# Optimization experiments

Hardware: AMD Instinct MI355X
Metric: run time of the kernel (lower is better)

## Reference

```python
import jax, jax.numpy as jnp
import numpy as np

N, L, C, NHEAD = 4, 2048, 1024, 8
D = C // NHEAD
EPS_ATTN = 1e-6
EPS_LN = 1e-5


def _w(key, shape, scale=0.02):
    return jax.random.normal(key, shape, dtype=jnp.float32) * scale


def setup_inputs() -> dict:
    key = jax.random.key(0)
    ks = jax.random.split(key, 32)
    inp = {
        'depth_feat': jax.random.normal(ks[0], (N, L, C), dtype=jnp.float32),
        'context_feat': jax.random.normal(ks[1], (N, L, C), dtype=jnp.float32),
        'depth_pos': jax.random.normal(ks[2], (N, L, C), dtype=jnp.float32),
        # encoder params (weights stored [in, out]; y = x @ W)
        'e_wq': _w(ks[3], (C, C)), 'e_wk': _w(ks[4], (C, C)), 'e_wv': _w(ks[5], (C, C)),
        'e_wm': _w(ks[6], (C, C)),
        'e_w1': _w(ks[7], (C, 2 * C)), 'e_w2': _w(ks[8], (2 * C, C)),
        'e_g1': jnp.ones((C,), jnp.float32), 'e_b1': jnp.zeros((C,), jnp.float32),
        'e_g2': jnp.ones((C,), jnp.float32), 'e_b2': jnp.zeros((C,), jnp.float32),
        # decoder params
        'd_wq0': _w(ks[9], (C, C)), 'd_wk0': _w(ks[10], (C, C)), 'd_wv0': _w(ks[11], (C, C)),
        'd_wm0': _w(ks[12], (C, C)),
        'd_wq1': _w(ks[13], (C, C)), 'd_wk1': _w(ks[14], (C, C)), 'd_wv1': _w(ks[15], (C, C)),
        'd_wm1': _w(ks[16], (C, C)),
        'd_w1': _w(ks[17], (C, 2 * C)), 'd_w2': _w(ks[18], (2 * C, C)),
        'd_g0': jnp.ones((C,), jnp.float32), 'd_b0': jnp.zeros((C,), jnp.float32),
        'd_g1': jnp.ones((C,), jnp.float32), 'd_b1': jnp.zeros((C,), jnp.float32),
        'd_g2': jnp.ones((C,), jnp.float32), 'd_b2': jnp.zeros((C,), jnp.float32),
    }
    return inp


def layernorm(x, g, b):
    m = jnp.mean(x, axis=-1, keepdims=True)
    v = jnp.mean(jnp.square(x - m), axis=-1, keepdims=True)
    return (x - m) * jax.lax.rsqrt(v + EPS_LN) * g + b


def linear_attention(q, k, v):
    # q,k,v: [N, L, H, D]; elu+1 feature map, O(L) kernelized attention
    Q = jax.nn.elu(q) + 1.0
    K = jax.nn.elu(k) + 1.0
    vlen = v.shape[1]
    v = v / vlen
    KV = jnp.einsum('nshd,nshv->nhdv', K, v)                    # [N,H,D,D]
    Z = 1.0 / (jnp.einsum('nlhd,nhd->nlh', Q, K.sum(axis=1)) + EPS_ATTN)
    out = jnp.einsum('nlhd,nhdv,nlh->nlhv', Q, KV, Z) * vlen    # [N,L,H,D]
    return out


def heads(x):
    n, l, c = x.shape
    return x.reshape(n, l, NHEAD, D)


def encoder_layer(x, wq, wk, wv, wm, w1, w2, g1, b1, g2, b2):
    n, l, c = x.shape
    msg = linear_attention(heads(x @ wq), heads(x @ wk), heads(x @ wv))
    msg = msg.reshape(n, l, c) @ wm
    x = x + layernorm(msg, g1, b1)
    x = x + layernorm(jax.nn.relu(x @ w1) @ w2, g2, b2)
    return x


def decoder_layer(x, src, wq0, wk0, wv0, wm0, wq1, wk1, wv1, wm1, w1, w2, g0, b0, g1, b1, g2, b2):
    n, l, c = x.shape
    msg = linear_attention(heads(x @ wq0), heads(x @ wk0), heads(x @ wv0))
    msg = msg.reshape(n, l, c) @ wm0
    x = x + layernorm(msg, g0, b0)
    msg = linear_attention(heads(x @ wq1), heads(src @ wk1), heads(src @ wv1))
    msg = msg.reshape(n, l, c) @ wm1
    x = x + layernorm(msg, g1, b1)
    x = x + layernorm(jax.nn.relu(x @ w1) @ w2, g2, b2)
    return x


def reference(depth_feat, context_feat, depth_pos,
              e_wq, e_wk, e_wv, e_wm, e_w1, e_w2, e_g1, e_b1, e_g2, e_b2,
              d_wq0, d_wk0, d_wv0, d_wm0, d_wq1, d_wk1, d_wv1, d_wm1,
              d_w1, d_w2, d_g0, d_b0, d_g1, d_b1, d_g2, d_b2):
    ctx = context_feat + depth_pos
    ctx = encoder_layer(ctx, e_wq, e_wk, e_wv, e_wm, e_w1, e_w2, e_g1, e_b1, e_g2, e_b2)
    out = decoder_layer(depth_feat, ctx,
                        d_wq0, d_wk0, d_wv0, d_wm0,
                        d_wq1, d_wk1, d_wv1, d_wm1,
                        d_w1, d_w2, d_g0, d_b0, d_g1, d_b1, d_g2, d_b2)
    return out
```

## Files before the change

kernel.cpp:

```cpp
#include <hip/hip_runtime.h>
#include <cstdint>

#define N_B 4
#define L_S 2048
#define C_F 1024
#define H_N 8
#define D_H 128
#define M_T (N_B * L_S)

typedef __bf16 bf16;
typedef __bf16 bf16x4 __attribute__((ext_vector_type(4)));
typedef __bf16 bf16x8 __attribute__((ext_vector_type(8)));
typedef float f32x4 __attribute__((ext_vector_type(4)));

typedef __attribute__((address_space(1))) void gvoid_t;
typedef __attribute__((address_space(3))) void lvoid_t;

__device__ __forceinline__ void lds_cp16(void* lds, const void* g) {
    __builtin_amdgcn_global_load_lds((gvoid_t*)g, (lvoid_t*)lds, 16, 0, 0);
}

__device__ __forceinline__ float elup1(float x) {
    return x > 0.0f ? x + 1.0f : __expf(x);
}

__device__ __forceinline__ void load4f(const void* base, size_t e0, int isbf, float* o) {
    if (isbf) {
        bf16x4 v = *(const bf16x4*)((const bf16*)base + e0);
        o[0] = (float)v[0]; o[1] = (float)v[1]; o[2] = (float)v[2]; o[3] = (float)v[3];
    } else {
        float4 v = *(const float4*)((const float*)base + e0);
        o[0] = v.x; o[1] = v.y; o[2] = v.z; o[3] = v.w;
    }
}

__global__ void detect_dtype(const unsigned int* g1, int* flag) {
    if (threadIdx.x == 0 && blockIdx.x == 0)
        *flag = (g1[0] == 0x3F803F80u) ? 1 : 0;
}

__global__ __launch_bounds__(256) void transpose_any(
        const void* __restrict__ src, bf16* __restrict__ dst,
        int R, int Cc, const int* __restrict__ flagp) {
    const int isbf = *flagp;
    __shared__ bf16 tile[32][33];
    const int bx = blockIdx.x * 32;
    const int by = blockIdx.y * 32;
    const int tx = threadIdx.x & 31;
    const int ty = threadIdx.x >> 5;
#pragma unroll
    for (int i = 0; i < 32; i += 8) {
        size_t ix = (size_t)(by + ty + i) * Cc + bx + tx;
        float v = isbf ? (float)((const bf16*)src)[ix] : ((const float*)src)[ix];
        tile[ty + i][tx] = (bf16)v;
    }
    __syncthreads();
#pragma unroll
    for (int i = 0; i < 32; i += 8)
        dst[(size_t)(bx + ty + i) * R + by + tx] = tile[tx][ty + i];
}

struct TAll {
    const void* src[16];
    unsigned int dstoff[16];
    int R[16];
    int C[16];
    int tile0[17];
};

__global__ __launch_bounds__(256) void transpose_all(
        TAll p, bf16* __restrict__ twall, const int* __restrict__ flagp) {
    const int isbf = *flagp;
    int gid = blockIdx.x;
    int w = 0;
    while (gid >= p.tile0[w + 1]) ++w;
    const int local = gid - p.tile0[w];
    const int R = p.R[w], Cc = p.C[w];
    const int tilesx = Cc >> 5;
    const int bx = (local % tilesx) * 32;
    const int by = (local / tilesx) * 32;
    const void* src = p.src[w];
    bf16* dst = twall + p.dstoff[w];
    __shared__ bf16 tile[32][33];
    const int tx = threadIdx.x & 31;
    const int ty = threadIdx.x >> 5;
#pragma unroll
    for (int i = 0; i < 32; i += 8) {
        size_t ix = (size_t)(by + ty + i) * Cc + bx + tx;
        float v = isbf ? (float)((const bf16*)src)[ix] : ((const float*)src)[ix];
        tile[ty + i][tx] = (bf16)v;
    }
    __syncthreads();
#pragma unroll
    for (int i = 0; i < 32; i += 8)
        dst[(size_t)(bx + ty + i) * R + by + tx] = tile[tx][ty + i];
}

template <int ACT>
__global__ __launch_bounds__(256, 2) void gemm_bt(
        const bf16* __restrict__ A, const bf16* __restrict__ Bt,
        bf16* __restrict__ C, int M, int N, int K) {
    __shared__ bf16 sA[128 * 64];
    __shared__ bf16 sB[128 * 64];
    const int t = threadIdx.x;
    const int lane = t & 63;
    const int w = t >> 6;
    const int wm = (w >> 1) * 64, wn = (w & 1) * 64;
    const int lr = lane & 15, lq = lane >> 4;
    const int m0 = blockIdx.y * 128, n0 = blockIdx.x * 128;

    f32x4 acc[4][4] = {};

    for (int kt = 0; kt < K; kt += 64) {
        const bf16* Ag = A + (size_t)m0 * K + kt;
        const bf16* Bg = Bt + (size_t)n0 * K + kt;
#pragma unroll
        for (int i = 0; i < 4; ++i) {
            int ci = t + i * 256;
            int r = ci >> 3, c8 = (ci & 7) * 8;
            lds_cp16(&sA[ci * 8], Ag + (size_t)r * K + c8);
        }
#pragma unroll
        for (int i = 0; i < 4; ++i) {
            int ci = t + i * 256;
            int r = ci >> 3, c8 = (ci & 7) * 8;
            lds_cp16(&sB[ci * 8], Bg + (size_t)r * K + c8);
        }
        __syncthreads();
#pragma unroll
        for (int kk = 0; kk < 64; kk += 32) {
            bf16x8 af[4], bfr[4];
#pragma unroll
            for (int mi = 0; mi < 4; ++mi)
                af[mi] = *(const bf16x8*)&sA[(wm + mi * 16 + lr) * 64 + kk + lq * 8];
#pragma unroll
            for (int ni = 0; ni < 4; ++ni)
                bfr[ni] = *(const bf16x8*)&sB[(wn + ni * 16 + lr) * 64 + kk + lq * 8];
#pragma unroll
            for (int mi = 0; mi < 4; ++mi)
#pragma unroll
                for (int ni = 0; ni < 4; ++ni)
                    acc[mi][ni] = __builtin_amdgcn_mfma_f32_16x16x32_bf16(
                        af[mi], bfr[ni], acc[mi][ni], 0, 0, 0);
        }
        __syncthreads();
    }
#pragma unroll
    for (int mi = 0; mi < 4; ++mi)
#pragma unroll
        for (int ni = 0; ni < 4; ++ni)
#pragma unroll
            for (int r = 0; r < 4; ++r) {
                int row = m0 + wm + mi * 16 + lq * 4 + r;
                int col = n0 + wn + ni * 16 + lr;
                float v = acc[mi][ni][r];
                if (ACT == 1) v = fmaxf(v, 0.0f);
                if (ACT == 2) v = v > 0.0f ? v + 1.0f : __expf(v);
                C[(size_t)row * N + col] = (bf16)v;
            }
}

#define STAGE_T(sarr, Gbase, ldstride, Tt)                                    \
    {                                                                         \
        const int sl_ = (Tt) & 3;                                             \
        _Pragma("unroll")                                                     \
        for (int i_ = 0; i_ < 2; ++i_) {                                      \
            int ci_ = t + i_ * 512;                                           \
            int r_ = ci_ >> 2, c8_ = (ci_ & 3) * 8;                           \
            lds_cp16(&sarr[sl_ * 8192 + ci_ * 8],                             \
                     (Gbase) + (size_t)r_ * (ldstride) + ((Tt) << 5) +        \
                         (c8_ ^ ((r_ & 3) << 3)));                            \
        }                                                                     \
    }

template <int ACT>
__global__ __launch_bounds__(512, 2) void gemm256(
        const bf16* __restrict__ A, const bf16* __restrict__ Bt,
        bf16* __restrict__ C, int M, int N, int K, int actsplit) {
    __shared__ bf16 sA[4 * 256 * 32];
    __shared__ bf16 sB[4 * 256 * 32];
    const int t = threadIdx.x;
    const int lane = t & 63;
    const int w = t >> 6;
    const int wr = w >> 2, wc = w & 3;
    const int lr = lane & 15, lq = lane >> 4;
    const int m0 = blockIdx.y * 256, n0 = blockIdx.x * 256;
    const int nt = K >> 5;

    const bf16* Ab = A + (size_t)m0 * K;
    const bf16* Bb = Bt + (size_t)n0 * K;

    f32x4 acc[8][4] = {};

    STAGE_T(sA, Ab, K, 0); STAGE_T(sB, Bb, K, 0);
    STAGE_T(sA, Ab, K, 1); STAGE_T(sB, Bb, K, 1);
    asm volatile("s_waitcnt vmcnt(4)" ::: "memory");
    __builtin_amdgcn_s_barrier();

    for (int T = 0; T < nt; ++T) {
        const bf16* sAs = &sA[(T & 3) * 8192];
        const bf16* sBs = &sB[(T & 3) * 8192];
        bf16x8 af[4], bfr[4], ag[4];
#pragma unroll
        for (int mi = 0; mi < 4; ++mi) {
            int row = wr * 128 + mi * 16 + lr;
            af[mi] = *(const bf16x8*)&sAs[row * 32 + ((lq * 8) ^ ((row & 3) << 3))];
        }
#pragma unroll
        for (int ni = 0; ni < 4; ++ni) {
            int row = wc * 64 + ni * 16 + lr;
            bfr[ni] = *(const bf16x8*)&sBs[row * 32 + ((lq * 8) ^ ((row & 3) << 3))];
        }
        if (T + 2 < nt) STAGE_T(sA, Ab, K, T + 2);
        __builtin_amdgcn_s_barrier();
        __builtin_amdgcn_s_setprio(1);
#pragma unroll
        for (int mi = 0; mi < 4; ++mi)
#pragma unroll
            for (int ni = 0; ni < 4; ++ni)
                acc[mi][ni] = __builtin_amdgcn_mfma_f32_16x16x32_bf16(
                    af[mi], bfr[ni], acc[mi][ni], 0, 0, 0);
        __builtin_amdgcn_s_setprio(0);
        __builtin_amdgcn_s_barrier();
#pragma unroll
        for (int mi = 0; mi < 4; ++mi) {
            int row = wr * 128 + (mi + 4) * 16 + lr;
            ag[mi] = *(const bf16x8*)&sAs[row * 32 + ((lq * 8) ^ ((row & 3) << 3))];
        }
        if (T + 2 < nt) STAGE_T(sB, Bb, K, T + 2);
        __builtin_amdgcn_s_barrier();
        __builtin_amdgcn_s_setprio(1);
#pragma unroll
        for (int mi = 0; mi < 4; ++mi)
#pragma unroll
            for (int ni = 0; ni < 4; ++ni)
                acc[mi + 4][ni] = __builtin_amdgcn_mfma_f32_16x16x32_bf16(
                    ag[mi], bfr[ni], acc[mi + 4][ni], 0, 0, 0);
        __builtin_amdgcn_s_setprio(0);
        if (T + 1 < nt) {
            if (T + 2 < nt) asm volatile("s_waitcnt vmcnt(4)" ::: "memory");
            else            asm volatile("s_waitcnt vmcnt(0)" ::: "memory");
        }
        __builtin_amdgcn_s_barrier();
    }
#pragma unroll
    for (int mi = 0; mi < 8; ++mi)
#pragma unroll
        for (int ni = 0; ni < 4; ++ni)
#pragma unroll
            for (int r = 0; r < 4; ++r) {
                int row = m0 + wr * 128 + mi * 16 + lq * 4 + r;
                int col = n0 + wc * 64 + ni * 16 + lr;
                float v = acc[mi][ni][r];
                if (ACT == 1) v = fmaxf(v, 0.0f);
                if (ACT == 3 && row < actsplit) v = v > 0.0f ? v + 1.0f : __expf(v);
                C[(size_t)row * N + col] = (bf16)v;
            }
}

__global__ __launch_bounds__(256, 2) void attn_kv_mfma(
        const bf16* __restrict__ ktg, const bf16* __restrict__ vtg,
        bf16* __restrict__ KVp, float* __restrict__ KSp) {
    const int nh = blockIdx.x;
    const int chunk = blockIdx.y;
    const int n = nh >> 3, h = nh & 7;
    const int t = threadIdx.x;
    const int lane = t & 63;
    const int w = t >> 6;
    const int wm = (w >> 1) * 64, wn = (w & 1) * 64;
    const int lr = lane & 15, lq = lane >> 4;
    __shared__ bf16 sA[128 * 64];
    __shared__ bf16 sB[128 * 64];
    const size_t base = (size_t)(h * D_H) * M_T + (size_t)n * L_S + chunk * 128;

    f32x4 acc[4][4] = {};
    float ks = 0.0f;
    const int dh = t >> 1, half = (t & 1) * 32;

    for (int kt = 0; kt < 128; kt += 64) {
        const bf16* Ag = vtg + base + kt;
        const bf16* Bg = ktg + base + kt;
#pragma unroll
        for (int i = 0; i < 4; ++i) {
            int ci = t + i * 256;
            int r = ci >> 3, c8 = (ci & 7) * 8;
            lds_cp16(&sA[ci * 8], Ag + (size_t)r * M_T + c8);
        }
#pragma unroll
        for (int i = 0; i < 4; ++i) {
            int ci = t + i * 256;
            int r = ci >> 3, c8 = (ci & 7) * 8;
            lds_cp16(&sB[ci * 8], Bg + (size_t)r * M_T + c8);
        }
        __syncthreads();
#pragma unroll
        for (int j = 0; j < 4; ++j) {
            bf16x8 v = *(const bf16x8*)&sB[dh * 64 + half + j * 8];
#pragma unroll
            for (int m = 0; m < 8; ++m) ks += (float)v[m];
        }
#pragma unroll
        for (int kk = 0; kk < 64; kk += 32) {
            bf16x8 af[4], bfr[4];
#pragma unroll
            for (int mi = 0; mi < 4; ++mi)
                af[mi] = *(const bf16x8*)&sA[(wm + mi * 16 + lr) * 64 + kk + lq * 8];
#pragma unroll
            for (int ni = 0; ni < 4; ++ni)
                bfr[ni] = *(const bf16x8*)&sB[(wn + ni * 16 + lr) * 64 + kk + lq * 8];
#pragma unroll
            for (int mi = 0; mi < 4; ++mi)
#pragma unroll
                for (int ni = 0; ni < 4; ++ni)
                    acc[mi][ni] = __builtin_amdgcn_mfma_f32_16x16x32_bf16(
                        af[mi], bfr[ni], acc[mi][ni], 0, 0, 0);
        }
        __syncthreads();
    }
    float ko = __shfl_xor(ks, 1);
    if (!(t & 1)) KSp[(nh * 16 + chunk) * D_H + dh] = ks + ko;

    bf16* out = KVp + ((size_t)(nh * 16 + chunk)) * (D_H * D_H);
#pragma unroll
    for (int mi = 0; mi < 4; ++mi)
#pragma unroll
        for (int ni = 0; ni < 4; ++ni)
#pragma unroll
            for (int r = 0; r < 4; ++r) {
                int row = wm + mi * 16 + lq * 4 + r;
                int col = wn + ni * 16 + lr;
                out[(size_t)row * D_H + col] = (bf16)acc[mi][ni][r];
            }
}

__global__ __launch_bounds__(256) void attn_reduce_t(
        const bf16* __restrict__ KVp, const float* __restrict__ KSp,
        bf16* __restrict__ KVt, float* __restrict__ Ksum) {
    const int nh = blockIdx.x;
    const int es = blockIdx.y;
    const int t = threadIdx.x;
    const size_t base = (size_t)nh * 16 * (D_H * D_H) + es * 4096 + t * 16;
    float fa[16] = {};
    for (int c = 0; c < 16; ++c) {
        const bf16* p = KVp + base + (size_t)c * (D_H * D_H);
        bf16x8 a = *(const bf16x8*)p;
        bf16x8 b = *(const bf16x8*)(p + 8);
#pragma unroll
        for (int m = 0; m < 8; ++m) { fa[m] += (float)a[m]; fa[8 + m] += (float)b[m]; }
    }
    bf16* o = KVt + (size_t)nh * (D_H * D_H) + es * 4096 + t * 16;
    bf16x8 oa, ob;
#pragma unroll
    for (int m = 0; m < 8; ++m) { oa[m] = (bf16)fa[m]; ob[m] = (bf16)fa[8 + m]; }
    *(bf16x8*)o = oa;
    *(bf16x8*)(o + 8) = ob;
    if (es == 0 && t < 128) {
        float s = 0.0f;
#pragma unroll
        for (int c = 0; c < 16; ++c) s += KSp[(nh * 16 + c) * D_H + t];
        Ksum[nh * D_H + t] = s;
    }
}

__global__ __launch_bounds__(256, 2) void attn_out_mfma(
        const bf16* __restrict__ qb, const bf16* __restrict__ KVt,
        const float* __restrict__ Ksum, bf16* __restrict__ ab) {
    const int nh = blockIdx.x, tile = blockIdx.y;
    const int n = nh >> 3, h = nh & 7;
    const int t = threadIdx.x;
    const int lane = t & 63;
    const int w = t >> 6;
    const int wm = (w >> 1) * 64, wn = (w & 1) * 64;
    const int lr = lane & 15, lq = lane >> 4;
    __shared__ bf16 sA[128 * 64];
    __shared__ bf16 sB[128 * 64];
    __shared__ float sKs[128];
    __shared__ float sZp[128][2];
    __shared__ float sZ[128];
    if (t < 128) sKs[t] = Ksum[nh * D_H + t];

    f32x4 acc[4][4] = {};
    float zacc = 0.0f;
    const int zrow = t >> 1, zoff = (t & 1) * 32;
    const size_t qbase = ((size_t)(n * L_S + tile * 128)) * C_F + h * D_H;

    for (int kt = 0; kt < 128; kt += 64) {
        __syncthreads();
#pragma unroll
        for (int i = 0; i < 4; ++i) {
            int ci = t + i * 256;
            int r = ci >> 3, c8 = (ci & 7) * 8;
            lds_cp16(&sA[ci * 8], qb + qbase + (size_t)r * C_F + kt + c8);
            lds_cp16(&sB[ci * 8], KVt + (size_t)nh * (D_H * D_H) + (size_t)r * D_H + kt + c8);
        }
        __syncthreads();
#pragma unroll 8
        for (int j = 0; j < 32; ++j)
            zacc += (float)sA[zrow * 64 + zoff + j] * sKs[kt + zoff + j];
#pragma unroll
        for (int kk = 0; kk < 64; kk += 32) {
            bf16x8 af[4], bfr[4];
#pragma unroll
            for (int mi = 0; mi < 4; ++mi)
                af[mi] = *(const bf16x8*)&sA[(wm + mi * 16 + lr) * 64 + kk + lq * 8];
#pragma unroll
            for (int ni = 0; ni < 4; ++ni)
                bfr[ni] = *(const bf16x8*)&sB[(wn + ni * 16 + lr) * 64 + kk + lq * 8];
#pragma unroll
            for (int mi = 0; mi < 4; ++mi)
#pragma unroll
                for (int ni = 0; ni < 4; ++ni)
                    acc[mi][ni] = __builtin_amdgcn_mfma_f32_16x16x32_bf16(
                        af[mi], bfr[ni], acc[mi][ni], 0, 0, 0);
        }
    }
    sZp[zrow][t & 1] = zacc;
    __syncthreads();
    if (t < 128) sZ[t] = 1.0f / (sZp[t][0] + sZp[t][1] + 1e-6f);
    __syncthreads();
#pragma unroll
    for (int mi = 0; mi < 4; ++mi)
#pragma unroll
        for (int ni = 0; ni < 4; ++ni)
#pragma unroll
            for (int r = 0; r < 4; ++r) {
                int row = wm + mi * 16 + lq * 4 + r;
                int col = wn + ni * 16 + lr;
                ab[qbase + (size_t)row * C_F + col] = (bf16)(acc[mi][ni][r] * sZ[row]);
            }
}

template <int F32OUT>
__global__ __launch_bounds__(256) void ln_res(
        const bf16* __restrict__ msg, const void* __restrict__ g,
        const void* __restrict__ bb, const int* __restrict__ flagp,
        const bf16* __restrict__ xin, void* __restrict__ xout) {
    const int isbf = *flagp;
    const int row = blockIdx.x * 4 + (threadIdx.x >> 6);
    const int lane = threadIdx.x & 63;
    const size_t base = (size_t)row * C_F;
    float m[16];
#pragma unroll
    for (int k = 0; k < 4; ++k) {
        bf16x4 v = *(const bf16x4*)(msg + base + k * 256 + lane * 4);
        m[k * 4 + 0] = (float)v[0]; m[k * 4 + 1] = (float)v[1];
        m[k * 4 + 2] = (float)v[2]; m[k * 4 + 3] = (float)v[3];
    }
    float s1 = 0.0f, s2 = 0.0f;
#pragma unroll
    for (int q = 0; q < 16; ++q) { s1 += m[q]; s2 += m[q] * m[q]; }
#pragma unroll
    for (int off = 32; off > 0; off >>= 1) {
        s1 += __shfl_down(s1, off);
        s2 += __shfl_down(s2, off);
    }
    s1 = __shfl(s1, 0);
    s2 = __shfl(s2, 0);
    const float mean = s1 / C_F;
    const float rs = rsqrtf(s2 / C_F - mean * mean + 1e-5f);
#pragma unroll
    for (int k = 0; k < 4; ++k) {
        const size_t cix = k * 256 + lane * 4;
        float ga[4], ba[4];
        load4f(g, cix, isbf, ga);
        load4f(bb, cix, isbf, ba);
        bf16x4 x4 = *(const bf16x4*)(xin + base + cix);
        if (F32OUT) {
            float4 of;
            of.x = (float)x4[0] + (m[k * 4 + 0] - mean) * rs * ga[0] + ba[0];
            of.y = (float)x4[1] + (m[k * 4 + 1] - mean) * rs * ga[1] + ba[1];
            of.z = (float)x4[2] + (m[k * 4 + 2] - mean) * rs * ga[2] + ba[2];
            of.w = (float)x4[3] + (m[k * 4 + 3] - mean) * rs * ga[3] + ba[3];
            *(float4*)((float*)xout + base + cix) = of;
        } else {
            bf16x4 ob;
            ob[0] = (bf16)((float)x4[0] + (m[k * 4 + 0] - mean) * rs * ga[0] + ba[0]);
            ob[1] = (bf16)((float)x4[1] + (m[k * 4 + 1] - mean) * rs * ga[1] + ba[1]);
            ob[2] = (bf16)((float)x4[2] + (m[k * 4 + 2] - mean) * rs * ga[2] + ba[2]);
            ob[3] = (bf16)((float)x4[3] + (m[k * 4 + 3] - mean) * rs * ga[3] + ba[3]);
            *(bf16x4*)((bf16*)xout + base + cix) = ob;
        }
    }
}

__global__ __launch_bounds__(256) void init_ctx_kernel(
        const void* __restrict__ a, const void* __restrict__ b,
        const int* __restrict__ flagp, bf16* __restrict__ xb) {
    const int isbf = *flagp;
    const size_t i = ((size_t)blockIdx.x * 256 + threadIdx.x) * 4;
    float av[4], bv[4];
    load4f(a, i, isbf, av);
    load4f(b, i, isbf, bv);
    bf16x4 o;
#pragma unroll
    for (int q = 0; q < 4; ++q) o[q] = (bf16)(av[q] + bv[q]);
    *(bf16x4*)(xb + i) = o;
}

__global__ __launch_bounds__(256) void conv_copy_kernel(
        const void* __restrict__ a, const int* __restrict__ flagp,
        bf16* __restrict__ xb) {
    const int isbf = *flagp;
    const size_t i = ((size_t)blockIdx.x * 256 + threadIdx.x) * 4;
    float av[4];
    load4f(a, i, isbf, av);
    bf16x4 o;
#pragma unroll
    for (int q = 0; q < 4; ++q) o[q] = (bf16)av[q];
    *(bf16x4*)(xb + i) = o;
}

extern "C" void kernel_launch(void* const* d_in, const int* in_sizes, int n_in,
                              void* d_out, int out_size, void* d_ws, size_t ws_size,
                              hipStream_t stream) {
    const size_t MB = 1u << 20;
    uint8_t* W = (uint8_t*)d_ws;
    bf16* xb    = (bf16*)(W + 0);
    bf16* ctxb  = (bf16*)(W + 16 * MB);
    bf16* qb    = (bf16*)(W + 32 * MB);
    bf16* kb    = (bf16*)(W + 48 * MB);
    bf16* vb    = (bf16*)(W + 64 * MB);
    bf16* hb    = kb;
    bf16* S     = (bf16*)(W + 80 * MB);
    bf16* TW    = (bf16*)(W + 96 * MB);
    bf16* KVp   = S;
    float* KSp  = (float*)(W + 100 * MB);
    bf16* KVt   = (bf16*)(W + 101 * MB);
    float* Ksum = (float*)(W + 102 * MB);
    int*   flag = (int*)(W + 102 * MB + 64 * 1024);
    bf16* TWall = (bf16*)(W + 104 * MB);
    const bool batched = (ws_size >= 145 * MB);

    detect_dtype<<<1, 64, 0, stream>>>((const unsigned int*)d_in[9], flag);

    const int widx[16] = {3,4,5,6,7,8,13,14,15,16,17,18,19,20,21,22};
    const int wR[16]   = {1024,1024,1024,1024,1024,2048,1024,1024,1024,1024,
                          1024,1024,1024,1024,1024,2048};
    const int wC[16]   = {1024,1024,1024,1024,2048,1024,1024,1024,1024,1024,
                          1024,1024,1024,1024,2048,1024};
    unsigned int off[16];
    {
        unsigned int acc = 0;
        for (int i = 0; i < 16; ++i) { off[i] = acc; acc += (unsigned int)wR[i] * wC[i]; }
    }
    if (batched) {
        TAll p;
        int tacc = 0;
        for (int i = 0; i < 16; ++i) {
            p.src[i] = d_in[widx[i]];
            p.dstoff[i] = off[i];
            p.R[i] = wR[i];
            p.C[i] = wC[i];
            p.tile0[i] = tacc;
            tacc += (wR[i] / 32) * (wC[i] / 32);
        }
        p.tile0[16] = tacc;
        transpose_all<<<tacc, 256, 0, stream>>>(p, TWall, flag);
    }
    auto SLOT = [&](int idx) {
        for (int i = 0; i < 16; ++i) if (widx[i] == idx) return i;
        return 0;
    };
    auto BT = [&](int idx) -> const bf16* {
        int s = SLOT(idx);
        if (batched) return TWall + off[s];
        dim3 g(wC[s] / 32, wR[s] / 32);
        transpose_any<<<g, 256, 0, stream>>>(d_in[idx], TW, wR[s], wC[s], flag);
        return TW;
    };
    auto TG = [&](int idx, const bf16* A, bf16* Cc, int Nn, int Kk, int act) {
        const bf16* Bt = BT(idx);
        dim3 g(Nn / 128, M_T / 128);
        if (act == 1)      gemm_bt<1><<<g, 256, 0, stream>>>(A, Bt, Cc, M_T, Nn, Kk);
        else if (act == 2) gemm_bt<2><<<g, 256, 0, stream>>>(A, Bt, Cc, M_T, Nn, Kk);
        else               gemm_bt<0><<<g, 256, 0, stream>>>(A, Bt, Cc, M_T, Nn, Kk);
    };
    auto KVF = [&](int kidx, int vidx, const bf16* X) {
        const bf16* Wt;
        if (batched) {
            Wt = TWall + off[SLOT(kidx)];
        } else {
            dim3 g(32, 32);
            transpose_any<<<g, 256, 0, stream>>>(d_in[kidx], TW, 1024, 1024, flag);
            transpose_any<<<g, 256, 0, stream>>>(d_in[vidx], TW + 1024 * 1024, 1024, 1024, flag);
            Wt = TW;
        }
        dim3 g(M_T / 256, (2 * C_F) / 256);
        gemm256<3><<<g, 512, 0, stream>>>(Wt, X, kb, 2 * C_F, M_T, C_F, C_F);
    };
    auto FFN1 = [&](int idx, const bf16* A) {
        const bf16* Bt = BT(idx);
        dim3 g((2 * C_F) / 256, M_T / 256);
        gemm256<1><<<g, 512, 0, stream>>>(A, Bt, hb, M_T, 2 * C_F, C_F, 0);
    };
    auto ATT = [&](const bf16* q, const bf16* k, const bf16* v, bf16* o) {
        attn_kv_mfma<<<dim3(32, 16), 256, 0, stream>>>(k, v, KVp, KSp);
        attn_reduce_t<<<dim3(32, 4), 256, 0, stream>>>(KVp, KSp, KVt, Ksum);
        attn_out_mfma<<<dim3(32, 16), 256, 0, stream>>>(q, KVt, Ksum, o);
    };
    auto LN = [&](const bf16* m, int gi, int bi, const bf16* xi, bf16* xo) {
        ln_res<0><<<M_T / 4, 256, 0, stream>>>(m, d_in[gi], d_in[bi], flag, xi, (void*)xo);
    };

    init_ctx_kernel<<<M_T * C_F / 1024, 256, 0, stream>>>(d_in[1], d_in[2], flag, xb);
    TG(3, xb, qb, C_F, C_F, 2);
    KVF(4, 5, xb);
    ATT(qb, kb, vb, S);
    TG(6, S, qb, C_F, C_F, 0);
    LN(qb, 9, 10, xb, xb);
    FFN1(7, xb);
    TG(8, hb, S, C_F, 2 * C_F, 0);
    LN(S, 11, 12, xb, ctxb);

    conv_copy_kernel<<<M_T * C_F / 1024, 256, 0, stream>>>(d_in[0], flag, xb);
    TG(13, xb, qb, C_F, C_F, 2);
    KVF(14, 15, xb);
    ATT(qb, kb, vb, S);
    TG(16, S, qb, C_F, C_F, 0);
    LN(qb, 23, 24, xb, xb);
    TG(17, xb, qb, C_F, C_F, 2);
    KVF(18, 19, ctxb);
    ATT(qb, kb, vb, S);
    TG(20, S, qb, C_F, C_F, 0);
    LN(qb, 25, 26, xb, xb);
    FFN1(21, xb);
    TG(22, hb, S, C_F, 2 * C_F, 0);
    ln_res<1><<<M_T / 4, 256, 0, stream>>>(S, d_in[27], d_in[28], flag, xb, d_out);
}
```

Measured before the change: 867.3 us.

## Replace 256-tile pipelined GEMM with 128x64 tiles and XCD-aware tile remap

Removes the 256x256 multi-stage pipelined GEMM and routes the KV-projection and FFN1 GEMMs through the simpler 128x128 kernel. N=1024 GEMMs now use a new 128x64-tile kernel that allows 4 blocks per CU. A tile_map function remaps workgroup IDs so neighbouring tiles land on the same XCD, aiming for better L2 reuse and more blocks in flight. The cost is losing the software-pipelined, LDS-swizzled 256 kernel, which may have had higher MFMA efficiency on the large GEMMs.

Result: slower. 927.7 us (+7.0%).

```diff
diff --git a/kernel.cpp b/kernel.cpp
--- a/kernel.cpp
+++ b/kernel.cpp
@@ -32,6 +32,18 @@
         float4 v = *(const float4*)((const float*)base + e0);
         o[0] = v.x; o[1] = v.y; o[2] = v.z; o[3] = v.w;
     }
+}
+
+__device__ __forceinline__ void tile_map(int orig, int gx, int gy,
+                                         int* mtile, int* ntile) {
+    const int nwg = gx * gy;
+    const int q = nwg >> 3;
+    const int s = (orig & 7) * q + (orig >> 3);
+    const int G = gx << 3;
+    const int g = s / G;
+    const int r = s - g * G;
+    *ntile = r >> 3;
+    *mtile = g * 8 + (r & 7);
 }
 
 __global__ void detect_dtype(const unsigned int* g1, int* flag) {
@@ -99,7 +111,7 @@
 template <int ACT>
 __global__ __launch_bounds__(256, 2) void gemm_bt(
         const bf16* __restrict__ A, const bf16* __restrict__ Bt,
-        bf16* __restrict__ C, int M, int N, int K) {
+        bf16* __restrict__ C, int M, int N, int K, int actsplit) {
     __shared__ bf16 sA[128 * 64];
     __shared__ bf16 sB[128 * 64];
     const int t = threadIdx.x;
@@ -107,24 +119,27 @@
     const int w = t >> 6;
     const int wm = (w >> 1) * 64, wn = (w & 1) * 64;
     const int lr = lane & 15, lq = lane >> 4;
-    const int m0 = blockIdx.y * 128, n0 = blockIdx.x * 128;
+    int mt, nt_;
+    tile_map(blockIdx.y * gridDim.x + blockIdx.x, gridDim.x, gridDim.y, &mt, &nt_);
+    const int m0 = mt * 128, n0 = nt_ * 128;
+
+    const bf16* Ab = A + (size_t)m0 * K;
+    const bf16* Bb = Bt + (size_t)n0 * K;
 
     f32x4 acc[4][4] = {};
 
     for (int kt = 0; kt < K; kt += 64) {
-        const bf16* Ag = A + (size_t)m0 * K + kt;
-        const bf16* Bg = Bt + (size_t)n0 * K + kt;
 #pragma unroll
         for (int i = 0; i < 4; ++i) {
             int ci = t + i * 256;
             int r = ci >> 3, c8 = (ci & 7) * 8;
-            lds_cp16(&sA[ci * 8], Ag + (size_t)r * K + c8);
+            lds_cp16(&sA[ci * 8], Ab + (size_t)r * K + kt + c8);
         }
 #pragma unroll
         for (int i = 0; i < 4; ++i) {
             int ci = t + i * 256;
             int r = ci >> 3, c8 = (ci & 7) * 8;
-            lds_cp16(&sB[ci * 8], Bg + (size_t)r * K + c8);
+            lds_cp16(&sB[ci * 8], Bb + (size_t)r * K + kt + c8);
         }
         __syncthreads();
 #pragma unroll
@@ -156,104 +171,74 @@
                 float v = acc[mi][ni][r];
                 if (ACT == 1) v = fmaxf(v, 0.0f);
                 if (ACT == 2) v = v > 0.0f ? v + 1.0f : __expf(v);
+                if (ACT == 3 && row < actsplit) v = v > 0.0f ? v + 1.0f : __expf(v);
                 C[(size_t)row * N + col] = (bf16)v;
             }
 }
 
-#define STAGE_T(sarr, Gbase, ldstride, Tt)                                    \
-    {                                                                         \
-        const int sl_ = (Tt) & 3;                                             \
-        _Pragma("unroll")                                                     \
-        for (int i_ = 0; i_ < 2; ++i_) {                                      \
-            int ci_ = t + i_ * 512;                                           \
-            int r_ = ci_ >> 2, c8_ = (ci_ & 3) * 8;                           \
-            lds_cp16(&sarr[sl_ * 8192 + ci_ * 8],                             \
-                     (Gbase) + (size_t)r_ * (ldstride) + ((Tt) << 5) +        \
-                         (c8_ ^ ((r_ & 3) << 3)));                            \
-        }                                                                     \
-    }
-
 template <int ACT>
-__global__ __launch_bounds__(512, 2) void gemm256(
+__global__ __launch_bounds__(256, 4) void gemm_bn64(
         const bf16* __restrict__ A, const bf16* __restrict__ Bt,
-        bf16* __restrict__ C, int M, int N, int K, int actsplit) {
-    __shared__ bf16 sA[4 * 256 * 32];
-    __shared__ bf16 sB[4 * 256 * 32];
+        bf16* __restrict__ C, int M, int N, int K) {
+    __shared__ bf16 sA[128 * 64];
+    __shared__ bf16 sB[64 * 64];
     const int t = threadIdx.x;
     const int lane = t & 63;
     const int w = t >> 6;
-    const int wr = w >> 2, wc = w & 3;
+    const int wm = (w >> 1) * 64, wn = (w & 1) * 32;
     const int lr = lane & 15, lq = lane >> 4;
-    const int m0 = blockIdx.y * 256, n0 = blockIdx.x * 256;
-    const int nt = K >> 5;
+    int mt, nt_;
+    tile_map(blockIdx.y * gridDim.x + blockIdx.x, gridDim.x, gridDim.y, &mt, &nt_);
+    const int m0 = mt * 128, n0 = nt_ * 64;
 
     const bf16* Ab = A + (size_t)m0 * K;
     const bf16* Bb = Bt + (size_t)n0 * K;
 
-    f32x4 acc[8][4] = {};
-
-    STAGE_T(sA, Ab, K, 0); STAGE_T(sB, Bb, K, 0);
-    STAGE_T(sA, Ab, K, 1); STAGE_T(sB, Bb, K, 1);
-    asm volatile("s_waitcnt vmcnt(4)" ::: "memory");
-    __builtin_amdgcn_s_barrier();
-
-    for (int T = 0; T < nt; ++T) {
-        const bf16* sAs = &sA[(T & 3) * 8192];
-        const bf16* sBs = &sB[(T & 3) * 8192];
-        bf16x8 af[4], bfr[4], ag[4];
-#pragma unroll
-        for (int mi = 0; mi < 4; ++mi) {
-            int row = wr * 128 + mi * 16 + lr;
-            af[mi] = *(const bf16x8*)&sAs[row * 32 + ((lq * 8) ^ ((row & 3) << 3))];
-        }
-#pragma unroll
-        for (int ni = 0; ni < 4; ++ni) {
-            int row = wc * 64 + ni * 16 + lr;
-            bfr[ni] = *(const bf16x8*)&sBs[row * 32 + ((lq * 8) ^ ((row & 3) << 3))];
-        }
-        if (T + 2 < nt) STAGE_T(sA, Ab, K, T + 2);
-        __builtin_amdgcn_s_barrier();
-        __builtin_amdgcn_s_setprio(1);
-#pragma unroll
-        for (int mi = 0; mi < 4; ++mi)
-#pragma unroll
-            for (int ni = 0; ni < 4; ++ni)
-                acc[mi][ni] = __builtin_amdgcn_mfma_f32_16x16x32_bf16(
-                    af[mi], bfr[ni], acc[mi][ni], 0, 0, 0);
-        __builtin_amdgcn_s_setprio(0);
-        __builtin_amdgcn_s_barrier();
-#pragma unroll
-        for (int mi = 0; mi < 4; ++mi) {
-            int row = wr * 128 + (mi + 4) * 16 + lr;
-            ag[mi] = *(const bf16x8*)&sAs[row * 32 + ((lq * 8) ^ ((row & 3) << 3))];
-        }
-        if (T + 2 < nt) STAGE_T(sB, Bb, K, T + 2);
-        __builtin_amdgcn_s_barrier();
-        __builtin_amdgcn_s_setprio(1);
-#pragma unroll
-        for (int mi = 0; mi < 4; ++mi)
-#pragma unroll
-            for (int ni = 0; ni < 4; ++ni)
-                acc[mi + 4][ni] = __builtin_amdgcn_mfma_f32_16x16x32_bf16(
-                    ag[mi], bfr[ni], acc[mi + 4][ni], 0, 0, 0);
-        __builtin_amdgcn_s_setprio(0);
-        if (T + 1 < nt) {
-            if (T + 2 < nt) asm volatile("s_waitcnt vmcnt(4)" ::: "memory");
-            else            asm volatile("s_waitcnt vmcnt(0)" ::: "memory");
-        }
-        __builtin_amdgcn_s_barrier();
-    }
-#pragma unroll
-    for (int mi = 0; mi < 8; ++mi)
-#pragma unroll
-        for (int ni = 0; ni < 4; ++ni)
+    f32x4 acc[4][2] = {};
+
+    for (int kt = 0; kt < K; kt += 64) {
+#pragma unroll
+        for (int i = 0; i < 4; ++i) {
+            int ci = t + i * 256;
+            int r = ci >> 3, c8 = (ci & 7) * 8;
+            lds_cp16(&sA[ci * 8], Ab + (size_t)r * K + kt + c8);
+        }
+#pragma unroll
+        for (int i = 0; i < 2; ++i) {
+            int ci = t + i * 256;
+            int r = ci >> 3, c8 = (ci & 7) * 8;
+            lds_cp16(&sB[ci * 8], Bb + (size_t)r * K + kt + c8);
+        }
+        __syncthreads();
+#pragma unroll
+        for (int kk = 0; kk < 64; kk += 32) {
+            bf16x8 af[4], bfr[2];
+#pragma unroll
+            for (int mi = 0; mi < 4; ++mi)
+                af[mi] = *(const bf16x8*)&sA[(wm + mi * 16 + lr) * 64 + kk + lq * 8];
+#pragma unroll
+            for (int ni = 0; ni < 2; ++ni)
+                bfr[ni] = *(const bf16x8*)&sB[(wn + ni * 16 + lr) * 64 + kk + lq * 8];
+#pragma unroll
+            for (int mi = 0; mi < 4; ++mi)
+#pragma unroll
+                for (int ni = 0; ni < 2; ++ni)
+                    acc[mi][ni] = __builtin_amdgcn_mfma_f32_16x16x32_bf16(
+                        af[mi], bfr[ni], acc[mi][ni], 0, 0, 0);
+        }
+        __syncthreads();
+    }
+#pragma unroll
+    for (int mi = 0; mi < 4; ++mi)
+#pragma unroll
+        for (int ni = 0; ni < 2; ++ni)
 #pragma unroll
             for (int r = 0; r < 4; ++r) {
-                int row = m0 + wr * 128 + mi * 16 + lq * 4 + r;
-                int col = n0 + wc * 64 + ni * 16 + lr;
+                int row = m0 + wm + mi * 16 + lq * 4 + r;
+                int col = n0 + wn + ni * 16 + lr;
                 float v = acc[mi][ni][r];
                 if (ACT == 1) v = fmaxf(v, 0.0f);
-                if (ACT == 3 && row < actsplit) v = v > 0.0f ? v + 1.0f : __expf(v);
+                if (ACT == 2) v = v > 0.0f ? v + 1.0f : __expf(v);
                 C[(size_t)row * N + col] = (bf16)v;
             }
 }
@@ -570,10 +555,17 @@
     };
     auto TG = [&](int idx, const bf16* A, bf16* Cc, int Nn, int Kk, int act) {
         const bf16* Bt = BT(idx);
-        dim3 g(Nn / 128, M_T / 128);
-        if (act == 1)      gemm_bt<1><<<g, 256, 0, stream>>>(A, Bt, Cc, M_T, Nn, Kk);
-        else if (act == 2) gemm_bt<2><<<g, 256, 0, stream>>>(A, Bt, Cc, M_T, Nn, Kk);
-        else               gemm_bt<0><<<g, 256, 0, stream>>>(A, Bt, Cc, M_T, Nn, Kk);
+        if (Nn == C_F) {
+            dim3 g(Nn / 64, M_T / 128);
+            if (act == 1)      gemm_bn64<1><<<g, 256, 0, stream>>>(A, Bt, Cc, M_T, Nn, Kk);
+            else if (act == 2) gemm_bn64<2><<<g, 256, 0, stream>>>(A, Bt, Cc, M_T, Nn, Kk);
+            else               gemm_bn64<0><<<g, 256, 0, stream>>>(A, Bt, Cc, M_T, Nn, Kk);
+        } else {
+            dim3 g(Nn / 128, M_T / 128);
+            if (act == 1)      gemm_bt<1><<<g, 256, 0, stream>>>(A, Bt, Cc, M_T, Nn, Kk, 0);
+            else if (act == 2) gemm_bt<2><<<g, 256, 0, stream>>>(A, Bt, Cc, M_T, Nn, Kk, 0);
+            else               gemm_bt<0><<<g, 256, 0, stream>>>(A, Bt, Cc, M_T, Nn, Kk, 0);
+        }
     };
     auto KVF = [&](int kidx, int vidx, const bf16* X) {
         const bf16* Wt;
@@ -585,13 +577,8 @@
             transpose_any<<<g, 256, 0, stream>>>(d_in[vidx], TW + 1024 * 1024, 1024, 1024, flag);
             Wt = TW;
         }
-        dim3 g(M_T / 256, (2 * C_F) / 256);
-        gemm256<3><<<g, 512, 0, stream>>>(Wt, X, kb, 2 * C_F, M_T, C_F, C_F);
-    };
-    auto FFN1 = [&](int idx, const bf16* A) {
-        const bf16* Bt = BT(idx);
-        dim3 g((2 * C_F) / 256, M_T / 256);
-        gemm256<1><<<g, 512, 0, stream>>>(A, Bt, hb, M_T, 2 * C_F, C_F, 0);
+        dim3 g(M_T / 128, (2 * C_F) / 128);
+        gemm_bt<3><<<g, 256, 0, stream>>>(Wt, X, kb, 2 * C_F, M_T, C_F, C_F);
     };
     auto ATT = [&](const bf16* q, const bf16* k, const bf16* v, bf16* o) {
         attn_kv_mfma<<<dim3(32, 16), 256, 0, stream>>>(k, v, KVp, KSp);
@@ -608,7 +595,7 @@
     ATT(qb, kb, vb, S);
     TG(6, S, qb, C_F, C_F, 0);
     LN(qb, 9, 10, xb, xb);
-    FFN1(7, xb);
+    TG(7, xb, hb, 2 * C_F, C_F, 1);
     TG(8, hb, S, C_F, 2 * C_F, 0);
     LN(S, 11, 12, xb, ctxb);
 
@@ -623,7 +610,7 @@
     ATT(qb, kb, vb, S);
     TG(20, S, qb, C_F, C_F, 0);
     LN(qb, 25, 26, xb, xb);
-    FFN1(21, xb);
+    TG(21, xb, hb, 2 * C_F, C_F, 1);
     TG(22, hb, S, C_F, 2 * C_F, 0);
     ln_res<1><<<M_T / 4, 256, 0, stream>>>(S, d_in[27], d_in[28], flag, xb, d_out);
 }
```
